# Kernel tuning notes

Measured on AMD Instinct MI355X. Metric: run time of the kernel, lower is better.

The kernel has to match this reference:

```python
import jax, jax.numpy as jnp
import numpy as np

D_MODEL = 40; N_LAYER = 256
D_INNER = 80; D_STATE = 16; D_CONV = 4; DT_RANK = 3  # mamba defaults: expand=2, dt_rank=ceil(40/16)
PE_HID = 48; FF_MULT = 4
B, L, N = 1, 400, 65536


def setup_inputs():
    key = jax.random.key(0)
    ks = jax.random.split(key, 16)
    f32 = jnp.float32
    def rn(k, shape, s=0.02):
        return jax.random.normal(k, shape, f32) * s
    inp = {}
    inp['mash_params'] = jax.random.normal(ks[0], (B, L, D_MODEL), f32)
    inp['qry'] = jax.random.uniform(ks[1], (B, N, 3), f32, -1.0, 1.0)
    # stacked per-layer Mamba params (leading dim = N_LAYER)
    inp['l_norm_w'] = jnp.ones((N_LAYER, D_MODEL), f32)
    inp['l_in_w'] = rn(ks[2], (N_LAYER, 2 * D_INNER, D_MODEL), 0.05)
    inp['l_conv_w'] = rn(ks[3], (N_LAYER, D_INNER, D_CONV), 0.2)
    inp['l_conv_b'] = jnp.zeros((N_LAYER, D_INNER), f32)
    inp['l_xproj_w'] = rn(ks[4], (N_LAYER, DT_RANK + 2 * D_STATE, D_INNER), 0.05)
    inp['l_dt_w'] = rn(ks[5], (N_LAYER, D_INNER, DT_RANK), 0.2)
    inp['l_dt_b'] = rn(ks[6], (N_LAYER, D_INNER), 0.5) - 4.0  # softplus -> small dt
    A = jnp.tile(jnp.arange(1, D_STATE + 1, dtype=f32)[None, None, :], (N_LAYER, D_INNER, 1))
    inp['l_A_log'] = jnp.log(A)
    inp['l_D'] = jnp.ones((N_LAYER, D_INNER), f32)
    inp['l_out_w'] = rn(ks[7], (N_LAYER, D_MODEL, D_INNER), 0.05)
    # PointEmbed MLP (Fourier basis is a fixed buffer, built in forward)
    inp['pe_mlp_w'] = rn(ks[8], (D_MODEL, PE_HID + 3), 0.1)
    inp['pe_mlp_b'] = jnp.zeros((D_MODEL,), f32)
    # PreNorm cross-attention (heads=1, dim_head=d_model)
    inp['ca_lnq_w'] = jnp.ones((D_MODEL,), f32); inp['ca_lnq_b'] = jnp.zeros((D_MODEL,), f32)
    inp['ca_lnc_w'] = jnp.ones((D_MODEL,), f32); inp['ca_lnc_b'] = jnp.zeros((D_MODEL,), f32)
    inp['ca_q_w'] = rn(ks[9], (D_MODEL, D_MODEL), 0.1)
    inp['ca_kv_w'] = rn(ks[10], (2 * D_MODEL, D_MODEL), 0.1)
    inp['ca_out_w'] = rn(ks[11], (D_MODEL, D_MODEL), 0.1)
    inp['ca_out_b'] = jnp.zeros((D_MODEL,), f32)
    # PreNorm GEGLU feed-forward
    inp['ff_ln_w'] = jnp.ones((D_MODEL,), f32); inp['ff_ln_b'] = jnp.zeros((D_MODEL,), f32)
    inp['ff_fc1_w'] = rn(ks[12], (2 * FF_MULT * D_MODEL, D_MODEL), 0.1)
    inp['ff_fc1_b'] = jnp.zeros((2 * FF_MULT * D_MODEL,), f32)
    inp['ff_fc2_w'] = rn(ks[13], (D_MODEL, FF_MULT * D_MODEL), 0.1)
    inp['ff_fc2_b'] = jnp.zeros((D_MODEL,), f32)
    inp['out_w'] = rn(ks[14], (1, D_MODEL), 0.1)
    inp['out_b'] = jnp.zeros((1,), f32)
    return inp


def _rmsnorm(x, w, eps=1e-5):
    return x * jax.lax.rsqrt(jnp.mean(x * x, -1, keepdims=True) + eps) * w


def _layernorm(x, w, b, eps=1e-5):
    m = jnp.mean(x, -1, keepdims=True)
    v = jnp.mean((x - m) ** 2, -1, keepdims=True)
    return (x - m) * jax.lax.rsqrt(v + eps) * w + b


def _mamba(u, p):
    # u: [b, l, d_model]
    xz = jnp.einsum('bld,ed->ble', u, p['in_w'])  # [b,l,2*di]
    x, z = jnp.split(xz, 2, -1)
    # depthwise causal conv1d, kernel D_CONV
    xt = jnp.swapaxes(x, 1, 2)  # [b, di, l]
    xc = jax.lax.conv_general_dilated(xt, p['conv_w'][:, None, :], (1,), [(D_CONV - 1, 0)],
                                      feature_group_count=D_INNER)
    x = jax.nn.silu(jnp.swapaxes(xc + p['conv_b'][None, :, None], 1, 2))  # [b,l,di]
    dbc = jnp.einsum('bld,ed->ble', x, p['xproj_w'])  # [b,l,dt_rank+2*ds]
    dtr = dbc[..., :DT_RANK]
    Bm = dbc[..., DT_RANK:DT_RANK + D_STATE]
    Cm = dbc[..., DT_RANK + D_STATE:]
    dt = jax.nn.softplus(jnp.einsum('blr,dr->bld', dtr, p['dt_w']) + p['dt_b'])  # [b,l,di]
    A = -jnp.exp(p['A_log'])  # [di, ds]
    dA = jnp.exp(dt[..., None] * A)                          # [b,l,di,ds]
    dBx = dt[..., None] * Bm[:, :, None, :] * x[..., None]   # [b,l,di,ds]
    def step(h, io):
        a, bx = io
        h = a * h + bx
        return h, h
    h0 = jnp.zeros((u.shape[0], D_INNER, D_STATE), u.dtype)
    _, hs = jax.lax.scan(step, h0, (jnp.moveaxis(dA, 1, 0), jnp.moveaxis(dBx, 1, 0)))
    hs = jnp.moveaxis(hs, 0, 1)  # [b,l,di,ds]
    y = jnp.einsum('blds,bls->bld', hs, Cm) + x * p['D']
    y = y * jax.nn.silu(z)
    return jnp.einsum('bld,ed->ble', y, p['out_w'])


def _forward(mash_params, qry, l_norm_w, l_in_w, l_conv_w, l_conv_b, l_xproj_w, l_dt_w, l_dt_b,
             l_A_log, l_D, l_out_w, pe_mlp_w, pe_mlp_b, ca_lnq_w, ca_lnq_b, ca_lnc_w, ca_lnc_b,
             ca_q_w, ca_kv_w, ca_out_w, ca_out_b, ff_ln_w, ff_ln_b, ff_fc1_w, ff_fc1_b,
             ff_fc2_w, ff_fc2_b, out_w, out_b):
    layer_params = dict(norm_w=l_norm_w, in_w=l_in_w, conv_w=l_conv_w, conv_b=l_conv_b,
                        xproj_w=l_xproj_w, dt_w=l_dt_w, dt_b=l_dt_b, A_log=l_A_log,
                        D=l_D, out_w=l_out_w)
    # Block: residual = x; h = RMSNorm(x); h = Mamba(h); then caller does x = h + residual
    def layer_fn(x, p):
        return x + _mamba(_rmsnorm(x, p['norm_w']), p), None
    x, _ = jax.lax.scan(layer_fn, mash_params, layer_params)
    # PointEmbed: Fourier features with fixed block-diagonal basis
    e = (2.0 ** jnp.arange(PE_HID // 6, dtype=jnp.float32)) * jnp.pi  # [8]
    z0 = jnp.zeros_like(e)
    basis = jnp.stack([jnp.concatenate([e, z0, z0]),
                       jnp.concatenate([z0, e, z0]),
                       jnp.concatenate([z0, z0, e])])  # [3, 24]
    proj = jnp.einsum('bnd,de->bne', qry, basis)
    pe = jnp.concatenate([jnp.sin(proj), jnp.cos(proj), qry], -1)  # [b,n,51]
    q_emb = jnp.einsum('bnf,df->bnd', pe, pe_mlp_w) + pe_mlp_b
    # PreNorm cross-attention (1 head, dim_head = d_model)
    qn = _layernorm(q_emb, ca_lnq_w, ca_lnq_b)
    cn = _layernorm(x, ca_lnc_w, ca_lnc_b)
    q = jnp.einsum('bnd,ed->bne', qn, ca_q_w)
    kv = jnp.einsum('bld,ed->ble', cn, ca_kv_w)
    k, v = jnp.split(kv, 2, -1)
    scale = D_MODEL ** -0.5
    attn = jax.nn.softmax(jnp.einsum('bnd,bld->bnl', q, k) * scale, axis=-1)  # [b,n,l]
    lat = jnp.einsum('bnl,bld->bnd', attn, v)
    lat = jnp.einsum('bnd,ed->bne', lat, ca_out_w) + ca_out_b
    # PreNorm GEGLU feed-forward with residual
    h = _layernorm(lat, ff_ln_w, ff_ln_b)
    a = jnp.einsum('bnd,ed->bne', h, ff_fc1_w) + ff_fc1_b
    x1, g = jnp.split(a, 2, -1)
    ff = jnp.einsum('bnf,df->bnd', x1 * jax.nn.gelu(g, approximate=False), ff_fc2_w) + ff_fc2_b
    lat = lat + ff
    occ = (jnp.einsum('bnd,od->bno', lat, out_w) + out_b)[..., 0]  # [b, n]
    return occ


def reference(mash_params, qry, l_norm_w, l_in_w, l_conv_w, l_conv_b, l_xproj_w, l_dt_w, l_dt_b,
              l_A_log, l_D, l_out_w, pe_mlp_w, pe_mlp_b, ca_lnq_w, ca_lnq_b, ca_lnc_w, ca_lnc_b,
              ca_q_w, ca_kv_w, ca_out_w, ca_out_b, ff_ln_w, ff_ln_b, ff_fc1_w, ff_fc1_b,
              ff_fc2_w, ff_fc2_b, out_w, out_b):
    return _forward(mash_params, qry, l_norm_w, l_in_w, l_conv_w, l_conv_b, l_xproj_w, l_dt_w,
                    l_dt_b, l_A_log, l_D, l_out_w, pe_mlp_w, pe_mlp_b, ca_lnq_w, ca_lnq_b,
                    ca_lnc_w, ca_lnc_b, ca_q_w, ca_kv_w, ca_out_w, ca_out_b, ff_ln_w, ff_ln_b,
                    ff_fc1_w, ff_fc1_b, ff_fc2_w, ff_fc2_b, out_w, out_b)
```

## Files before the change

### kernel.cpp

```cpp
#include <hip/hip_runtime.h>


#define CH 4
#define NCHUNK 100
#define TPB1 320

typedef unsigned long long u64;

__device__ __forceinline__ u64 pack2(float a, float b) {
  return ((u64)__float_as_uint(b) << 32) | (u64)__float_as_uint(a);
}
__device__ __forceinline__ float unplo(u64 a) {
  return __uint_as_float((unsigned)a);
}
__device__ __forceinline__ float unphi(u64 a) {
  return __uint_as_float((unsigned)(a >> 32));
}

__global__ void init_flags(int* __restrict__ flags) {
  int i = blockIdx.x * 256 + threadIdx.x;
  if (i < 256 * 16) flags[i] = 0;
}

__global__ __launch_bounds__(TPB1) void mamba_pipe(
    const float* __restrict__ mash,
    const float* __restrict__ g_norm_w,
    const float* __restrict__ g_in_w,
    const float* __restrict__ g_conv_w,
    const float* __restrict__ g_conv_b,
    const float* __restrict__ g_xp_w,
    const float* __restrict__ g_dt_w,
    const float* __restrict__ g_dt_b,
    const float* __restrict__ g_alog,
    const float* __restrict__ g_D,
    const float* __restrict__ g_out_w,
    float* __restrict__ xb0,
    float* __restrict__ xb1,
    int* __restrict__ flags,
    const float* __restrict__ qry,
    const float* __restrict__ pe_w, const float* __restrict__ pe_b,
    const float* __restrict__ lnq_w, const float* __restrict__ lnq_b,
    const float* __restrict__ qw,
    float* __restrict__ qstore)
{
  const int tid = threadIdx.x;

  if (blockIdx.x >= 256) {
    const int n = (blockIdx.x - 256) * TPB1 + tid;
    if (n < 65536) {
      const float qx = qry[n * 3 + 0], qy = qry[n * 3 + 1], qz = qry[n * 3 + 2];
      float qe[40];
#pragma unroll
      for (int d = 0; d < 40; ++d) qe[d] = pe_b[d];
#pragma unroll 1
      for (int j = 0; j < 8; ++j) {
        float f = 3.14159265358979323846f * (float)(1 << j);
        float sx, cx, sy, cy, sz, cz;
        __sincosf(qx * f, &sx, &cx);
        __sincosf(qy * f, &sy, &cy);
        __sincosf(qz * f, &sz, &cz);
#pragma unroll
        for (int d = 0; d < 40; ++d) {
          const float* r = pe_w + d * 51;
          qe[d] += sx * r[j] + sy * r[j + 8] + sz * r[j + 16]
                 + cx * r[j + 24] + cy * r[j + 32] + cz * r[j + 40];
        }
      }
#pragma unroll
      for (int d = 0; d < 40; ++d) {
        const float* r = pe_w + d * 51;
        qe[d] += qx * r[48] + qy * r[49] + qz * r[50];
      }
      float qn[40];
      {
        float m = 0.f;
#pragma unroll
        for (int d = 0; d < 40; ++d) m += qe[d];
        m *= (1.f / 40.f);
        float var = 0.f;
#pragma unroll
        for (int d = 0; d < 40; ++d) { float dv = qe[d] - m; var += dv * dv; }
        float rstd = rsqrtf(var * (1.f / 40.f) + 1e-5f);
#pragma unroll
        for (int d = 0; d < 40; ++d)
          qn[d] = (qe[d] - m) * rstd * lnq_w[d] + lnq_b[d];
      }
      float q[40];
#pragma unroll
      for (int e = 0; e < 40; ++e) {
        const float* r = qw + e * 40;
        float s = 0.f;
#pragma unroll
        for (int d = 0; d < 40; ++d) s += qn[d] * r[d];
        q[e] = s;
      }
#pragma unroll
      for (int e = 0; e < 40; ++e) qstore[e * 65536 + n] = q[e];
    }
    return;
  }

  const int layer = blockIdx.x;

  __shared__ float xin[160];
  __shared__ float xz[640];
  __shared__ float xs[320];
  __shared__ float dbc[144];
  __shared__ float yb[320];
  __shared__ float xhist[240];

  const int e_in = tid % 160;
  const int tA = tid / 160;
  float w_in_r[40];
  {
    const float4* g = (const float4*)(g_in_w + layer * 6400 + e_in * 40);
    const float4* nw = (const float4*)(g_norm_w + layer * 40);
#pragma unroll
    for (int k = 0; k < 10; ++k) {
      float4 v = g[k];
      float4 n = nw[k];
      w_in_r[4 * k] = v.x * n.x; w_in_r[4 * k + 1] = v.y * n.y;
      w_in_r[4 * k + 2] = v.z * n.z; w_in_r[4 * k + 3] = v.w * n.w;
    }
  }
  const int d_c = tid % 80;
  const int t_c = tid / 80;
  float cw[4]; float cb;
  {
    float4 v = *(const float4*)(g_conv_w + layer * 320 + d_c * 4);
    cw[0] = v.x; cw[1] = v.y; cw[2] = v.z; cw[3] = v.w;
    cb = g_conv_b[layer * 80 + d_c];
  }
  const int halfp = tid & 1;
  const int p_x = tid >> 1;
  const int t_x = p_x / 35, e_x = p_x % 35;
  float w_xp_r[40];
  if (p_x < 140) {
    const float4* g = (const float4*)(g_xp_w + layer * 2800 + e_x * 80 + halfp * 40);
#pragma unroll
    for (int k = 0; k < 10; ++k) {
      float4 v = g[k];
      w_xp_r[4 * k] = v.x; w_xp_r[4 * k + 1] = v.y;
      w_xp_r[4 * k + 2] = v.z; w_xp_r[4 * k + 3] = v.w;
    }
  }
  const int d_ch = tid >> 2;
  const int qq = tid & 3;
  float negA[4], hst[4];
  {
    float4 v = *(const float4*)(g_alog + layer * 1280 + tid * 4);
    negA[0] = -__expf(v.x); negA[1] = -__expf(v.y);
    negA[2] = -__expf(v.z); negA[3] = -__expf(v.w);
    hst[0] = hst[1] = hst[2] = hst[3] = 0.f;
  }
  const float dtw0 = g_dt_w[layer * 240 + d_ch * 3 + 0];
  const float dtw1 = g_dt_w[layer * 240 + d_ch * 3 + 1];
  const float dtw2 = g_dt_w[layer * 240 + d_ch * 3 + 2];
  const float dtb = g_dt_b[layer * 80 + d_ch];
  const float wD = g_D[layer * 80 + d_ch];
  const int p_o = tid >> 1;
  const int t_o = p_o / 40, e_o = p_o % 40;
  float w_out_r[40];
  {
    const float4* g = (const float4*)(g_out_w + layer * 3200 + e_o * 80 + halfp * 40);
#pragma unroll
    for (int k = 0; k < 10; ++k) {
      float4 v = g[k];
      w_out_r[4 * k] = v.x; w_out_r[4 * k + 1] = v.y;
      w_out_r[4 * k + 2] = v.z; w_out_r[4 * k + 3] = v.w;
    }
  }

  for (int i = tid; i < 240; i += TPB1) xhist[i] = 0.f;
  __syncthreads();

  const float* src = (layer == 0) ? mash : ((layer & 1) ? xb0 : xb1);
  float* dst = (layer & 1) ? xb1 : xb0;
  int* flag_prev = flags + (layer - 1) * 16;
  int* flag_cur = flags + layer * 16;

  for (int c = 0; c < NCHUNK; ++c) {
    const int t0 = c * CH;

    if (layer == 0) {
#pragma unroll
      for (int tt = 0; tt < 2; ++tt) {
        const int t = tA + 2 * tt;
        const float4* sp = (const float4*)(src + (t0 + t) * 40);
        float ss = 0.f, sd = 0.f;
#pragma unroll
        for (int k = 0; k < 10; ++k) {
          float4 v = sp[k];
          ss += v.x * v.x + v.y * v.y + v.z * v.z + v.w * v.w;
          sd += w_in_r[4 * k] * v.x + w_in_r[4 * k + 1] * v.y
              + w_in_r[4 * k + 2] * v.z + w_in_r[4 * k + 3] * v.w;
        }
        xz[t * 160 + e_in] = sd * rsqrtf(ss * (1.f / 40.f) + 1e-5f);
      }
      if (tid < 160) xin[tid] = src[t0 * 40 + tid];
    } else {
      while (__hip_atomic_load(flag_prev, __ATOMIC_RELAXED,
                               __HIP_MEMORY_SCOPE_AGENT) <= c)
        __builtin_amdgcn_s_sleep(1);
#pragma unroll
      for (int tt = 0; tt < 2; ++tt) {
        const int t = tA + 2 * tt;
        const u64* sp = (const u64*)(src + (t0 + t) * 40);
        float ss = 0.f, sd = 0.f;
#pragma unroll
        for (int k = 0; k < 20; ++k) {
          u64 a = __hip_atomic_load(sp + k, __ATOMIC_RELAXED,
                                    __HIP_MEMORY_SCOPE_AGENT);
          float v0 = unplo(a), v1 = unphi(a);
          ss += v0 * v0 + v1 * v1;
          sd += w_in_r[2 * k] * v0 + w_in_r[2 * k + 1] * v1;
        }
        xz[t * 160 + e_in] = sd * rsqrtf(ss * (1.f / 40.f) + 1e-5f);
      }
      if (tid < 80) {
        u64 a = __hip_atomic_load((const u64*)(src + t0 * 40) + tid,
                                  __ATOMIC_RELAXED, __HIP_MEMORY_SCOPE_AGENT);
        xin[2 * tid] = unplo(a);
        xin[2 * tid + 1] = unphi(a);
      }
    }
    __syncthreads();

    {
      float acc = cb;
#pragma unroll
      for (int j = 0; j < 4; ++j) {
        int lt = t_c - 3 + j;
        float xv = (lt >= 0) ? xz[lt * 160 + d_c] : xhist[(lt + 3) * 80 + d_c];
        acc += cw[j] * xv;
      }
      xs[t_c * 80 + d_c] = acc / (1.f + __expf(-acc));
    }
    __syncthreads();

    if (p_x < 140) {
      const float4* xp = (const float4*)&xs[t_x * 80 + halfp * 40];
      float s = 0.f;
#pragma unroll
      for (int k = 0; k < 10; ++k) {
        float4 v = xp[k];
        s += w_xp_r[4 * k] * v.x + w_xp_r[4 * k + 1] * v.y
           + w_xp_r[4 * k + 2] * v.z + w_xp_r[4 * k + 3] * v.w;
      }
      s += __shfl_xor(s, 1);
      if (halfp == 0) dbc[t_x * 36 + e_x] = s;
    } else {
      for (int k = tid - 280; k < 240; k += 40)
        xhist[k] = xz[(1 + k / 80) * 160 + (k % 80)];
    }
    __syncthreads();

#pragma unroll
    for (int t = 0; t < CH; ++t) {
      const float* db = &dbc[t * 36];
      float sdt = dtb + db[0] * dtw0 + db[1] * dtw1 + db[2] * dtw2;
      float dtval = (sdt > 15.f) ? sdt : __logf(1.f + __expf(sdt));
      float xval = xs[t * 80 + d_ch];
      float part = 0.f;
#pragma unroll
      for (int j = 0; j < 4; ++j) {
        int s_i = qq * 4 + j;
        float Bv = db[3 + s_i];
        float Cv = db[19 + s_i];
        hst[j] = __expf(dtval * negA[j]) * hst[j] + dtval * Bv * xval;
        part += hst[j] * Cv;
      }
      part += __shfl_xor(part, 1);
      part += __shfl_xor(part, 2);
      if (qq == 0) {
        float yv = part + xval * wD;
        float z = xz[t * 160 + 80 + d_ch];
        yb[t * 80 + d_ch] = yv * z / (1.f + __expf(-z));
      }
    }
    __syncthreads();

    {
      const float4* yp = (const float4*)&yb[t_o * 80 + halfp * 40];
      float s = 0.f;
#pragma unroll
      for (int k = 0; k < 10; ++k) {
        float4 v = yp[k];
        s += w_out_r[4 * k] * v.x + w_out_r[4 * k + 1] * v.y
           + w_out_r[4 * k + 2] * v.z + w_out_r[4 * k + 3] * v.w;
      }
      s += __shfl_xor(s, 1);
      float r = xin[p_o] + s;
      float r2 = __shfl_xor(r, 2);
      if ((tid & 3) == 0)
        __hip_atomic_store((u64*)(dst + t0 * 40 + p_o), pack2(r, r2),
                           __ATOMIC_RELAXED, __HIP_MEMORY_SCOPE_AGENT);
    }
    __syncthreads();
    if (tid == 0)
      __hip_atomic_store(flag_cur, c + 1, __ATOMIC_RELAXED,
                         __HIP_MEMORY_SCOPE_AGENT);
  }
}

__global__ __launch_bounds__(64) void kv_kernel(
    const float* __restrict__ xfin,
    const float* __restrict__ lnc_w, const float* __restrict__ lnc_b,
    const float* __restrict__ kv_w,
    float* __restrict__ kbuf, float* __restrict__ vbuf)
{
  int t = blockIdx.x;
  int lane = threadIdx.x;
  float x = (lane < 40) ? xfin[t * 40 + lane] : 0.f;
  float s = x;
#pragma unroll
  for (int o = 32; o >= 1; o >>= 1) s += __shfl_xor(s, o);
  float m = s * (1.f / 40.f);
  float dv = (lane < 40) ? (x - m) : 0.f;
  float v2 = dv * dv;
#pragma unroll
  for (int o = 32; o >= 1; o >>= 1) v2 += __shfl_xor(v2, o);
  float rstd = rsqrtf(v2 * (1.f / 40.f) + 1e-5f);
  __shared__ float cn[40];
  if (lane < 40) cn[lane] = dv * rstd * lnc_w[lane] + lnc_b[lane];
  __syncthreads();
  for (int e = lane; e < 80; e += 64) {
    float acc = 0.f;
#pragma unroll
    for (int d = 0; d < 40; ++d) acc += cn[d] * kv_w[e * 40 + d];
    if (e < 40) kbuf[t * 40 + e] = acc;
    else vbuf[t * 40 + (e - 40)] = acc;
  }
}

__global__ __launch_bounds__(256) void query_fast(
    const float* __restrict__ qstore,
    const float* __restrict__ ow, const float* __restrict__ ob,
    const float* __restrict__ flw, const float* __restrict__ flb,
    const float* __restrict__ w1, const float* __restrict__ b1,
    const float* __restrict__ w2, const float* __restrict__ b2,
    const float* __restrict__ outw, const float* __restrict__ outb,
    const float* __restrict__ kbuf, const float* __restrict__ vbuf,
    float* __restrict__ out)
{
  const int tid = threadIdx.x;
  const int h = __builtin_amdgcn_readfirstlane((tid >> 6) & 3);
  const int lane = tid & 63;
  const int n = blockIdx.x * 64 + lane;
  const int p1 = tid ^ 64, p2 = tid ^ 128, p3 = tid ^ 192;
  __shared__ float colbuf[40 * 256];

  float q[40];
#pragma unroll
  for (int e = 0; e < 40; ++e) q[e] = qstore[e * 65536 + n];

  float acc[40];
#pragma unroll
  for (int d = 0; d < 40; ++d) acc[d] = 0.f;
  float mx = -1e30f, l = 0.f;
  const float scale = 0.15811388300841897f;
  const int tbeg = h * 100;
#pragma unroll 1
  for (int t = tbeg; t < tbeg + 100; t += 2) {
    const float4* ka = (const float4*)(kbuf + t * 40);
    const float4* kb = (const float4*)(kbuf + t * 40 + 40);
    float a0 = 0.f, a1 = 0.f, b0 = 0.f, b1s = 0.f;
#pragma unroll
    for (int k = 0; k < 10; ++k) {
      float4 k4 = ka[k];
      float4 j4 = kb[k];
      a0 += q[4 * k] * k4.x + q[4 * k + 1] * k4.y;
      a1 += q[4 * k + 2] * k4.z + q[4 * k + 3] * k4.w;
      b0 += q[4 * k] * j4.x + q[4 * k + 1] * j4.y;
      b1s += q[4 * k + 2] * j4.z + q[4 * k + 3] * j4.w;
    }
    float sa = (a0 + a1) * scale;
    float sb = (b0 + b1s) * scale;
    {
      if (sa > mx) {
        float corr = __expf(mx - sa);
        l *= corr;
#pragma unroll
        for (int d = 0; d < 40; ++d) acc[d] *= corr;
        mx = sa;
      }
      float p = __expf(sa - mx);
      l += p;
      const float4* vr = (const float4*)(vbuf + t * 40);
#pragma unroll
      for (int k = 0; k < 10; ++k) {
        float4 v4 = vr[k];
        acc[4 * k] += p * v4.x; acc[4 * k + 1] += p * v4.y;
        acc[4 * k + 2] += p * v4.z; acc[4 * k + 3] += p * v4.w;
      }
    }
    {
      if (sb > mx) {
        float corr = __expf(mx - sb);
        l *= corr;
#pragma unroll
        for (int d = 0; d < 40; ++d) acc[d] *= corr;
        mx = sb;
      }
      float p = __expf(sb - mx);
      l += p;
      const float4* vr = (const float4*)(vbuf + (t + 1) * 40);
#pragma unroll
      for (int k = 0; k < 10; ++k) {
        float4 v4 = vr[k];
        acc[4 * k] += p * v4.x; acc[4 * k + 1] += p * v4.y;
        acc[4 * k + 2] += p * v4.z; acc[4 * k + 3] += p * v4.w;
      }
    }
  }

  {
    float* redm = colbuf;
    float* redl = colbuf + 256;
    redm[tid] = mx; redl[tid] = l;
  }
  __syncthreads();
  float a0c, a1c, a2c, a3c, linv;
  {
    float m1 = colbuf[p1], m2 = colbuf[p2], m3 = colbuf[p3];
    float l1 = colbuf[256 + p1], l2 = colbuf[256 + p2], l3 = colbuf[256 + p3];
    float nm = fmaxf(fmaxf(mx, m1), fmaxf(m2, m3));
    a0c = __expf(mx - nm); a1c = __expf(m1 - nm);
    a2c = __expf(m2 - nm); a3c = __expf(m3 - nm);
    float L = l * a0c + l1 * a1c + l2 * a2c + l3 * a3c;
    linv = 1.f / L;
  }
  __syncthreads();
#pragma unroll
  for (int d = 0; d < 40; ++d) colbuf[d * 256 + tid] = acc[d];
  __syncthreads();
  float lat[40];
#pragma unroll
  for (int d = 0; d < 40; ++d)
    lat[d] = (acc[d] * a0c + colbuf[d * 256 + p1] * a1c
            + colbuf[d * 256 + p2] * a2c + colbuf[d * 256 + p3] * a3c) * linv;
  __syncthreads();

  float lath[10];
#pragma unroll
  for (int dd = 0; dd < 10; ++dd) {
    float v = lat[dd];
    v = (h == 1) ? lat[dd + 10] : v;
    v = (h == 2) ? lat[dd + 20] : v;
    v = (h == 3) ? lat[dd + 30] : v;
    lath[dd] = v;
  }
  float lp[40];
#pragma unroll
  for (int e = 0; e < 40; ++e) lp[e] = 0.f;
#pragma unroll 1
  for (int dd = 0; dd < 10; ++dd) {
    const float lv = lath[dd];
    const int d = h * 10 + dd;
#pragma unroll
    for (int e = 0; e < 40; ++e) lp[e] += lv * ow[e * 40 + d];
  }
#pragma unroll
  for (int e = 0; e < 40; ++e) colbuf[e * 256 + tid] = lp[e];
  __syncthreads();
  float lat2[40];
#pragma unroll
  for (int e = 0; e < 40; ++e)
    lat2[e] = ob[e] + lp[e] + colbuf[e * 256 + p1]
            + colbuf[e * 256 + p2] + colbuf[e * 256 + p3];
  __syncthreads();

  float hh[40];
  {
    float m = 0.f;
#pragma unroll
    for (int d = 0; d < 40; ++d) m += lat2[d];
    m *= (1.f / 40.f);
    float var = 0.f;
#pragma unroll
    for (int d = 0; d < 40; ++d) { float dv = lat2[d] - m; var += dv * dv; }
    float rstd = rsqrtf(var * (1.f / 40.f) + 1e-5f);
#pragma unroll
    for (int d = 0; d < 40; ++d) hh[d] = (lat2[d] - m) * rstd * flw[d] + flb[d];
  }
  float ff[40];
#pragma unroll
  for (int d = 0; d < 40; ++d) ff[d] = 0.f;
#pragma unroll 1
  for (int ee = 0; ee < 40; ++ee) {
    const int e = h * 40 + ee;
    const float* r1 = w1 + e * 40;
    const float* r2 = w1 + (160 + e) * 40;
    float s0 = 0.f, s1 = 0.f;
#pragma unroll
    for (int d = 0; d < 40; ++d) { s0 += hh[d] * r1[d]; s1 += hh[d] * r2[d]; }
    float x1 = s0 + b1[e];
    float g = s1 + b1[160 + e];
    float tv = x1 * (0.5f * g * (1.f + erff(g * 0.70710678118654752f)));
#pragma unroll
    for (int d = 0; d < 40; ++d) ff[d] += tv * w2[d * 160 + e];
  }
#pragma unroll
  for (int d = 0; d < 40; ++d) colbuf[d * 256 + tid] = ff[d];
  __syncthreads();
  float r = outb[0];
#pragma unroll
  for (int d = 0; d < 40; ++d) {
    float f = ff[d] + colbuf[d * 256 + p1] + colbuf[d * 256 + p2]
            + colbuf[d * 256 + p3] + b2[d];
    r += (lat2[d] + f) * outw[d];
  }
  if (h == 0) out[n] = r;
}

__global__ __launch_bounds__(256) void query_kernel_fb(
    const float* __restrict__ qry,
    const float* __restrict__ pe_w, const float* __restrict__ pe_b,
    const float* __restrict__ lnq_w, const float* __restrict__ lnq_b,
    const float* __restrict__ qw,
    const float* __restrict__ ow, const float* __restrict__ ob,
    const float* __restrict__ flw, const float* __restrict__ flb,
    const float* __restrict__ w1, const float* __restrict__ b1,
    const float* __restrict__ w2, const float* __restrict__ b2,
    const float* __restrict__ outw, const float* __restrict__ outb,
    const float* __restrict__ kbuf, const float* __restrict__ vbuf,
    float* __restrict__ out)
{
  const int tid = threadIdx.x;
  const int h = __builtin_amdgcn_readfirstlane((tid >> 6) & 1);
  const int pj = tid >> 7;
  const int lane = tid & 63;
  const int n = blockIdx.x * 128 + pj * 64 + lane;
  const int ptn = tid ^ 64;
  __shared__ float colbuf[40 * 256];
  __shared__ float redm[256], redl[256];

  const float qx = qry[n * 3 + 0], qy = qry[n * 3 + 1], qz = qry[n * 3 + 2];
  float qp[40];
#pragma unroll
  for (int d = 0; d < 40; ++d) qp[d] = 0.f;
#pragma unroll
  for (int jj = 0; jj < 4; ++jj) {
    const int j = h * 4 + jj;
    float f = 3.14159265358979323846f * (float)(1 << j);
    float sx, cx, sy, cy, sz, cz;
    __sincosf(qx * f, &sx, &cx);
    __sincosf(qy * f, &sy, &cy);
    __sincosf(qz * f, &sz, &cz);
#pragma unroll
    for (int d = 0; d < 40; ++d) {
      const float* r = pe_w + d * 51;
      qp[d] += sx * r[j] + sy * r[j + 8] + sz * r[j + 16]
             + cx * r[j + 24] + cy * r[j + 32] + cz * r[j + 40];
    }
  }
#pragma unroll
  for (int d = 0; d < 40; ++d) colbuf[d * 256 + tid] = qp[d];
  __syncthreads();
  float qe[40];
#pragma unroll
  for (int d = 0; d < 40; ++d) {
    const float* r = pe_w + d * 51;
    qe[d] = pe_b[d] + qp[d] + colbuf[d * 256 + ptn]
          + qx * r[48] + qy * r[49] + qz * r[50];
  }
  __syncthreads();
  float qn[40];
  {
    float m = 0.f;
#pragma unroll
    for (int d = 0; d < 40; ++d) m += qe[d];
    m *= (1.f / 40.f);
    float var = 0.f;
#pragma unroll
    for (int d = 0; d < 40; ++d) { float dv = qe[d] - m; var += dv * dv; }
    float rstd = rsqrtf(var * (1.f / 40.f) + 1e-5f);
#pragma unroll
    for (int d = 0; d < 40; ++d) qn[d] = (qe[d] - m) * rstd * lnq_w[d] + lnq_b[d];
  }
  float qnh[20];
#pragma unroll
  for (int dd = 0; dd < 20; ++dd) qnh[dd] = h ? qn[dd + 20] : qn[dd];
  float q[40];
#pragma unroll
  for (int e = 0; e < 40; ++e) q[e] = 0.f;
#pragma unroll 1
  for (int dd = 0; dd < 20; ++dd) {
    const float qv = qnh[dd];
    const int d = h * 20 + dd;
#pragma unroll
    for (int e = 0; e < 40; ++e) q[e] += qv * qw[e * 40 + d];
  }
#pragma unroll
  for (int e = 0; e < 40; ++e) colbuf[e * 256 + tid] = q[e];
  __syncthreads();
#pragma unroll
  for (int e = 0; e < 40; ++e) q[e] += colbuf[e * 256 + ptn];
  __syncthreads();

  float acc[40];
#pragma unroll
  for (int d = 0; d < 40; ++d) acc[d] = 0.f;
  float mx = -1e30f, l = 0.f;
  const float scale = 0.15811388300841897f;
  const int tbeg = h * 200, tend = tbeg + 200;
#pragma unroll 1
  for (int t = tbeg; t < tend; ++t) {
    const float4* kr = (const float4*)(kbuf + t * 40);
    float s0 = 0.f, s1 = 0.f, s2 = 0.f, s3 = 0.f;
#pragma unroll
    for (int k = 0; k < 10; ++k) {
      float4 k4 = kr[k];
      s0 += q[4 * k] * k4.x; s1 += q[4 * k + 1] * k4.y;
      s2 += q[4 * k + 2] * k4.z; s3 += q[4 * k + 3] * k4.w;
    }
    float s = ((s0 + s1) + (s2 + s3)) * scale;
    if (s > mx) {
      float corr = __expf(mx - s);
      l *= corr;
#pragma unroll
      for (int d = 0; d < 40; ++d) acc[d] *= corr;
      mx = s;
    }
    float p = __expf(s - mx);
    l += p;
    const float4* vr = (const float4*)(vbuf + t * 40);
#pragma unroll
    for (int k = 0; k < 10; ++k) {
      float4 v4 = vr[k];
      acc[4 * k] += p * v4.x; acc[4 * k + 1] += p * v4.y;
      acc[4 * k + 2] += p * v4.z; acc[4 * k + 3] += p * v4.w;
    }
  }
#pragma unroll
  for (int d = 0; d < 40; ++d) colbuf[d * 256 + tid] = acc[d];
  redm[tid] = mx; redl[tid] = l;
  __syncthreads();
  float lat[40];
  {
    float m2 = redm[ptn];
    float l2 = redl[ptn];
    float nm = fmaxf(mx, m2);
    float a = __expf(mx - nm), b = __expf(m2 - nm);
    float lm = l * a + l2 * b;
    float linv = 1.f / lm;
#pragma unroll
    for (int d = 0; d < 40; ++d)
      lat[d] = (acc[d] * a + colbuf[d * 256 + ptn] * b) * linv;
  }
  __syncthreads();
  float lath[20];
#pragma unroll
  for (int dd = 0; dd < 20; ++dd) lath[dd] = h ? lat[dd + 20] : lat[dd];
  float lp[40];
#pragma unroll
  for (int e = 0; e < 40; ++e) lp[e] = 0.f;
#pragma unroll 1
  for (int dd = 0; dd < 20; ++dd) {
    const float lv = lath[dd];
    const int d = h * 20 + dd;
#pragma unroll
    for (int e = 0; e < 40; ++e) lp[e] += lv * ow[e * 40 + d];
  }
#pragma unroll
  for (int e = 0; e < 40; ++e) colbuf[e * 256 + tid] = lp[e];
  __syncthreads();
  float lat2[40];
#pragma unroll
  for (int e = 0; e < 40; ++e) lat2[e] = ob[e] + lp[e] + colbuf[e * 256 + ptn];
  __syncthreads();
  float hh[40];
  {
    float m = 0.f;
#pragma unroll
    for (int d = 0; d < 40; ++d) m += lat2[d];
    m *= (1.f / 40.f);
    float var = 0.f;
#pragma unroll
    for (int d = 0; d < 40; ++d) { float dv = lat2[d] - m; var += dv * dv; }
    float rstd = rsqrtf(var * (1.f / 40.f) + 1e-5f);
#pragma unroll
    for (int d = 0; d < 40; ++d) hh[d] = (lat2[d] - m) * rstd * flw[d] + flb[d];
  }
  float ff[40];
#pragma unroll
  for (int d = 0; d < 40; ++d) ff[d] = 0.f;
#pragma unroll 1
  for (int ee = 0; ee < 80; ++ee) {
    const int e = h * 80 + ee;
    const float* r1 = w1 + e * 40;
    const float* r2 = w1 + (160 + e) * 40;
    float s0 = 0.f, s1 = 0.f;
#pragma unroll
    for (int d = 0; d < 40; ++d) { s0 += hh[d] * r1[d]; s1 += hh[d] * r2[d]; }
    float x1 = s0 + b1[e];
    float g = s1 + b1[160 + e];
    float tv = x1 * (0.5f * g * (1.f + erff(g * 0.70710678118654752f)));
#pragma unroll
    for (int d = 0; d < 40; ++d) ff[d] += tv * w2[d * 160 + e];
  }
#pragma unroll
  for (int d = 0; d < 40; ++d) colbuf[d * 256 + tid] = ff[d];
  __syncthreads();
  float r = outb[0];
#pragma unroll
  for (int d = 0; d < 40; ++d) {
    float f = ff[d] + colbuf[d * 256 + ptn] + b2[d];
    r += (lat2[d] + f) * outw[d];
  }
  if (h == 0) out[n] = r;
}

extern "C" void kernel_launch(void* const* d_in, const int* in_sizes, int n_in,
                              void* d_out, int out_size, void* d_ws, size_t ws_size,
                              hipStream_t stream) {
  const float* mash   = (const float*)d_in[0];
  const float* qry    = (const float*)d_in[1];
  const float* lnw    = (const float*)d_in[2];
  const float* linw   = (const float*)d_in[3];
  const float* lconvw = (const float*)d_in[4];
  const float* lconvb = (const float*)d_in[5];
  const float* lxpw   = (const float*)d_in[6];
  const float* ldtw   = (const float*)d_in[7];
  const float* ldtb   = (const float*)d_in[8];
  const float* lAlog  = (const float*)d_in[9];
  const float* lD     = (const float*)d_in[10];
  const float* loutw  = (const float*)d_in[11];
  const float* pew    = (const float*)d_in[12];
  const float* peb    = (const float*)d_in[13];
  const float* lnqw   = (const float*)d_in[14];
  const float* lnqb   = (const float*)d_in[15];
  const float* lncw   = (const float*)d_in[16];
  const float* lncb   = (const float*)d_in[17];
  const float* qw     = (const float*)d_in[18];
  const float* kvw    = (const float*)d_in[19];
  const float* oww    = (const float*)d_in[20];
  const float* owb    = (const float*)d_in[21];
  const float* flnw   = (const float*)d_in[22];
  const float* flnb   = (const float*)d_in[23];
  const float* w1     = (const float*)d_in[24];
  const float* b1     = (const float*)d_in[25];
  const float* w2     = (const float*)d_in[26];
  const float* b2     = (const float*)d_in[27];
  const float* outw   = (const float*)d_in[28];
  const float* outb   = (const float*)d_in[29];

  float* wsf = (float*)d_ws;
  float* xb0 = wsf;
  float* xb1 = wsf + 16000;
  float* kbuf = wsf + 32000;
  float* vbuf = wsf + 48000;
  int* flags = (int*)(wsf + 64000);
  float* qstore = wsf + 68096;
  const size_t needed = (size_t)68096 * 4 + (size_t)40 * 65536 * 4;
  const bool pre = ws_size >= needed;

  hipLaunchKernelGGL(init_flags, dim3(16), dim3(256), 0, stream, flags);
  hipLaunchKernelGGL(mamba_pipe, dim3(pre ? 461 : 256), dim3(TPB1), 0, stream,
                     mash, lnw, linw, lconvw, lconvb, lxpw, ldtw, ldtb, lAlog,
                     lD, loutw, xb0, xb1, flags,
                     qry, pew, peb, lnqw, lnqb, qw, qstore);
  hipLaunchKernelGGL(kv_kernel, dim3(400), dim3(64), 0, stream,
                     xb1, lncw, lncb, kvw, kbuf, vbuf);
  if (pre) {
    hipLaunchKernelGGL(query_fast, dim3(1024), dim3(256), 0, stream,
                       qstore, oww, owb, flnw, flnb,
                       w1, b1, w2, b2, outw, outb, kbuf, vbuf, (float*)d_out);
  } else {
    hipLaunchKernelGGL(query_kernel_fb, dim3(512), dim3(256), 0, stream,
                       qry, pew, peb, lnqw, lnqb, qw, oww, owb, flnw, flnb,
                       w1, b1, w2, b2, outw, outb, kbuf, vbuf, (float*)d_out);
  }
}
```

Baseline: 2.113 ms.

## Fuse KV projection and query attention into the Mamba pipeline via flag-driven streaming

Adds 205 extra blocks to the persistent mamba_pipe kernel. They wait until point-embedding blocks publish q, then consume each final-layer output chunk as soon as its flag advances, computing LayerNorm and the K/V projection on the fly and running online-softmax attention and the feed-forward tail per query. This removes the separate kv_kernel and query_fast launches and overlaps query work with the serial 256-layer scan. In exchange it relies on spin-waiting blocks being co-resident with the producer blocks. Each thread also now does the whole FFN and output projection alone rather than splitting it across four waves, so per-thread compute rises.

Result: no change. 2.151 ms (+1.8%).

```diff
diff --git a/kernel.cpp b/kernel.cpp
--- a/kernel.cpp
+++ b/kernel.cpp
@@ -4,6 +4,8 @@
 #define CH 4
 #define NCHUNK 100
 #define TPB1 320
+#define NPE 205
+#define NQA 205
 
 typedef unsigned long long u64;
 
@@ -41,11 +43,19 @@
     const float* __restrict__ pe_w, const float* __restrict__ pe_b,
     const float* __restrict__ lnq_w, const float* __restrict__ lnq_b,
     const float* __restrict__ qw,
-    float* __restrict__ qstore)
+    float* __restrict__ qstore,
+    const float* __restrict__ lnc_w, const float* __restrict__ lnc_b,
+    const float* __restrict__ kv_w,
+    const float* __restrict__ ow, const float* __restrict__ ob,
+    const float* __restrict__ flw, const float* __restrict__ flb,
+    const float* __restrict__ w1, const float* __restrict__ b1,
+    const float* __restrict__ w2, const float* __restrict__ b2,
+    const float* __restrict__ outw, const float* __restrict__ outb,
+    float* __restrict__ out)
 {
   const int tid = threadIdx.x;
 
-  if (blockIdx.x >= 256) {
+  if (blockIdx.x >= 256 && blockIdx.x < 256 + NPE) {
     const int n = (blockIdx.x - 256) * TPB1 + tid;
     if (n < 65536) {
       const float qx = qry[n * 3 + 0], qy = qry[n * 3 + 1], qz = qry[n * 3 + 2];
@@ -95,8 +105,162 @@
         q[e] = s;
       }
 #pragma unroll
-      for (int e = 0; e < 40; ++e) qstore[e * 65536 + n] = q[e];
-    }
+      for (int e = 0; e < 40; ++e)
+        __hip_atomic_store(&qstore[e * 65536 + n], q[e],
+                           __ATOMIC_RELAXED, __HIP_MEMORY_SCOPE_AGENT);
+    }
+    __syncthreads();
+    if (tid == 0)
+      __hip_atomic_fetch_add(flags + 4088, 1,
+                             __ATOMIC_RELAXED, __HIP_MEMORY_SCOPE_AGENT);
+    return;
+  }
+
+  if (blockIdx.x >= 256 + NPE) {
+    const int n = (blockIdx.x - 256 - NPE) * TPB1 + tid;
+    const bool qvalid = (n < 65536);
+    const int w = tid >> 6;
+    const int lane = tid & 63;
+    __shared__ __align__(16) float kvx[160];
+    __shared__ __align__(16) float cns[4][40];
+    __shared__ __align__(16) float ks[4][40];
+    __shared__ __align__(16) float vs[4][40];
+
+    int* pe_done = flags + 4088;
+    int* flag255 = flags + 255 * 16;
+
+    while (__hip_atomic_load(pe_done, __ATOMIC_RELAXED,
+                             __HIP_MEMORY_SCOPE_AGENT) < NPE)
+      __builtin_amdgcn_s_sleep(32);
+
+    float q[40];
+#pragma unroll
+    for (int e = 0; e < 40; ++e)
+      q[e] = qvalid ? __hip_atomic_load(&qstore[e * 65536 + n],
+                                        __ATOMIC_RELAXED,
+                                        __HIP_MEMORY_SCOPE_AGENT) : 0.f;
+
+    float acc[40];
+#pragma unroll
+    for (int d = 0; d < 40; ++d) acc[d] = 0.f;
+    float mx = -1e30f, l = 0.f;
+    const float scale = 0.15811388300841897f;
+
+#pragma unroll 1
+    for (int c = 0; c < NCHUNK; ++c) {
+      while (__hip_atomic_load(flag255, __ATOMIC_RELAXED,
+                               __HIP_MEMORY_SCOPE_AGENT) <= c)
+        __builtin_amdgcn_s_sleep(32);
+      if (tid < 80) {
+        u64 a = __hip_atomic_load((const u64*)(xb1 + c * 160) + tid,
+                                  __ATOMIC_RELAXED, __HIP_MEMORY_SCOPE_AGENT);
+        kvx[2 * tid] = unplo(a);
+        kvx[2 * tid + 1] = unphi(a);
+      }
+      __syncthreads();
+      {
+        float x = (w < 4 && lane < 40) ? kvx[w * 40 + lane] : 0.f;
+        float s = x;
+#pragma unroll
+        for (int o = 32; o >= 1; o >>= 1) s += __shfl_xor(s, o);
+        float m = s * (1.f / 40.f);
+        float dv = (lane < 40) ? (x - m) : 0.f;
+        float v2 = dv * dv;
+#pragma unroll
+        for (int o = 32; o >= 1; o >>= 1) v2 += __shfl_xor(v2, o);
+        float rstd = rsqrtf(v2 * (1.f / 40.f) + 1e-5f);
+        if (w < 4 && lane < 40)
+          cns[w][lane] = dv * rstd * lnc_w[lane] + lnc_b[lane];
+      }
+      __syncthreads();
+      if (w < 4) {
+        for (int e = lane; e < 80; e += 64) {
+          float a = 0.f;
+#pragma unroll
+          for (int d = 0; d < 40; ++d) a += cns[w][d] * kv_w[e * 40 + d];
+          if (e < 40) ks[w][e] = a;
+          else vs[w][e - 40] = a;
+        }
+      }
+      __syncthreads();
+#pragma unroll 1
+      for (int t = 0; t < 4; ++t) {
+        const float4* kr = (const float4*)&ks[t][0];
+        float s0 = 0.f, s1 = 0.f, s2 = 0.f, s3 = 0.f;
+#pragma unroll
+        for (int k = 0; k < 10; ++k) {
+          float4 k4 = kr[k];
+          s0 += q[4 * k] * k4.x; s1 += q[4 * k + 1] * k4.y;
+          s2 += q[4 * k + 2] * k4.z; s3 += q[4 * k + 3] * k4.w;
+        }
+        float s = ((s0 + s1) + (s2 + s3)) * scale;
+        if (s > mx) {
+          float corr = __expf(mx - s);
+          l *= corr;
+#pragma unroll
+          for (int d = 0; d < 40; ++d) acc[d] *= corr;
+          mx = s;
+        }
+        float p = __expf(s - mx);
+        l += p;
+        const float4* vr = (const float4*)&vs[t][0];
+#pragma unroll
+        for (int k = 0; k < 10; ++k) {
+          float4 v4 = vr[k];
+          acc[4 * k] += p * v4.x; acc[4 * k + 1] += p * v4.y;
+          acc[4 * k + 2] += p * v4.z; acc[4 * k + 3] += p * v4.w;
+        }
+      }
+      __syncthreads();
+    }
+
+    float linv = 1.f / l;
+#pragma unroll
+    for (int d = 0; d < 40; ++d) acc[d] *= linv;
+    float lat2[40];
+#pragma unroll 1
+    for (int e = 0; e < 40; ++e) {
+      const float* r = ow + e * 40;
+      float s = 0.f;
+#pragma unroll
+      for (int d = 0; d < 40; ++d) s += acc[d] * r[d];
+      lat2[e] = ob[e] + s;
+    }
+    float hh[40];
+    {
+      float m = 0.f;
+#pragma unroll
+      for (int d = 0; d < 40; ++d) m += lat2[d];
+      m *= (1.f / 40.f);
+      float var = 0.f;
+#pragma unroll
+      for (int d = 0; d < 40; ++d) { float dv = lat2[d] - m; var += dv * dv; }
+      float rstd = rsqrtf(var * (1.f / 40.f) + 1e-5f);
+#pragma unroll
+      for (int d = 0; d < 40; ++d)
+        hh[d] = (lat2[d] - m) * rstd * flw[d] + flb[d];
+    }
+    float ff[40];
+#pragma unroll
+    for (int d = 0; d < 40; ++d) ff[d] = 0.f;
+#pragma unroll 1
+    for (int e = 0; e < 160; ++e) {
+      const float* r1 = w1 + e * 40;
+      const float* r2 = w1 + (160 + e) * 40;
+      float s0 = 0.f, s1 = 0.f;
+#pragma unroll
+      for (int d = 0; d < 40; ++d) { s0 += hh[d] * r1[d]; s1 += hh[d] * r2[d]; }
+      float x1 = s0 + b1[e];
+      float g = s1 + b1[160 + e];
+      float tv = x1 * (0.5f * g * (1.f + erff(g * 0.70710678118654752f)));
+#pragma unroll
+      for (int d = 0; d < 40; ++d) ff[d] += tv * w2[d * 160 + e];
+    }
+    float r = outb[0];
+#pragma unroll
+    for (int d = 0; d < 40; ++d)
+      r += (lat2[d] + ff[d] + b2[d]) * outw[d];
+    if (qvalid) out[n] = r;
     return;
   }
 
@@ -331,186 +495,6 @@
     if (e < 40) kbuf[t * 40 + e] = acc;
     else vbuf[t * 40 + (e - 40)] = acc;
   }
-}
-
-__global__ __launch_bounds__(256) void query_fast(
-    const float* __restrict__ qstore,
-    const float* __restrict__ ow, const float* __restrict__ ob,
-    const float* __restrict__ flw, const float* __restrict__ flb,
-    const float* __restrict__ w1, const float* __restrict__ b1,
-    const float* __restrict__ w2, const float* __restrict__ b2,
-    const float* __restrict__ outw, const float* __restrict__ outb,
-    const float* __restrict__ kbuf, const float* __restrict__ vbuf,
-    float* __restrict__ out)
-{
-  const int tid = threadIdx.x;
-  const int h = __builtin_amdgcn_readfirstlane((tid >> 6) & 3);
-  const int lane = tid & 63;
-  const int n = blockIdx.x * 64 + lane;
-  const int p1 = tid ^ 64, p2 = tid ^ 128, p3 = tid ^ 192;
-  __shared__ float colbuf[40 * 256];
-
-  float q[40];
-#pragma unroll
-  for (int e = 0; e < 40; ++e) q[e] = qstore[e * 65536 + n];
-
-  float acc[40];
-#pragma unroll
-  for (int d = 0; d < 40; ++d) acc[d] = 0.f;
-  float mx = -1e30f, l = 0.f;
-  const float scale = 0.15811388300841897f;
-  const int tbeg = h * 100;
-#pragma unroll 1
-  for (int t = tbeg; t < tbeg + 100; t += 2) {
-    const float4* ka = (const float4*)(kbuf + t * 40);
-    const float4* kb = (const float4*)(kbuf + t * 40 + 40);
-    float a0 = 0.f, a1 = 0.f, b0 = 0.f, b1s = 0.f;
-#pragma unroll
-    for (int k = 0; k < 10; ++k) {
-      float4 k4 = ka[k];
-      float4 j4 = kb[k];
-      a0 += q[4 * k] * k4.x + q[4 * k + 1] * k4.y;
-      a1 += q[4 * k + 2] * k4.z + q[4 * k + 3] * k4.w;
-      b0 += q[4 * k] * j4.x + q[4 * k + 1] * j4.y;
-      b1s += q[4 * k + 2] * j4.z + q[4 * k + 3] * j4.w;
-    }
-    float sa = (a0 + a1) * scale;
-    float sb = (b0 + b1s) * scale;
-    {
-      if (sa > mx) {
-        float corr = __expf(mx - sa);
-        l *= corr;
-#pragma unroll
-        for (int d = 0; d < 40; ++d) acc[d] *= corr;
-        mx = sa;
-      }
-      float p = __expf(sa - mx);
-      l += p;
-      const float4* vr = (const float4*)(vbuf + t * 40);
-#pragma unroll
-      for (int k = 0; k < 10; ++k) {
-        float4 v4 = vr[k];
-        acc[4 * k] += p * v4.x; acc[4 * k + 1] += p * v4.y;
-        acc[4 * k + 2] += p * v4.z; acc[4 * k + 3] += p * v4.w;
-      }
-    }
-    {
-      if (sb > mx) {
-        float corr = __expf(mx - sb);
-        l *= corr;
-#pragma unroll
-        for (int d = 0; d < 40; ++d) acc[d] *= corr;
-        mx = sb;
-      }
-      float p = __expf(sb - mx);
-      l += p;
-      const float4* vr = (const float4*)(vbuf + (t + 1) * 40);
-#pragma unroll
-      for (int k = 0; k < 10; ++k) {
-        float4 v4 = vr[k];
-        acc[4 * k] += p * v4.x; acc[4 * k + 1] += p * v4.y;
-        acc[4 * k + 2] += p * v4.z; acc[4 * k + 3] += p * v4.w;
-      }
-    }
-  }
-
-  {
-    float* redm = colbuf;
-    float* redl = colbuf + 256;
-    redm[tid] = mx; redl[tid] = l;
-  }
-  __syncthreads();
-  float a0c, a1c, a2c, a3c, linv;
-  {
-    float m1 = colbuf[p1], m2 = colbuf[p2], m3 = colbuf[p3];
-    float l1 = colbuf[256 + p1], l2 = colbuf[256 + p2], l3 = colbuf[256 + p3];
-    float nm = fmaxf(fmaxf(mx, m1), fmaxf(m2, m3));
-    a0c = __expf(mx - nm); a1c = __expf(m1 - nm);
-    a2c = __expf(m2 - nm); a3c = __expf(m3 - nm);
-    float L = l * a0c + l1 * a1c + l2 * a2c + l3 * a3c;
-    linv = 1.f / L;
-  }
-  __syncthreads();
-#pragma unroll
-  for (int d = 0; d < 40; ++d) colbuf[d * 256 + tid] = acc[d];
-  __syncthreads();
-  float lat[40];
-#pragma unroll
-  for (int d = 0; d < 40; ++d)
-    lat[d] = (acc[d] * a0c + colbuf[d * 256 + p1] * a1c
-            + colbuf[d * 256 + p2] * a2c + colbuf[d * 256 + p3] * a3c) * linv;
-  __syncthreads();
-
-  float lath[10];
-#pragma unroll
-  for (int dd = 0; dd < 10; ++dd) {
-    float v = lat[dd];
-    v = (h == 1) ? lat[dd + 10] : v;
-    v = (h == 2) ? lat[dd + 20] : v;
-    v = (h == 3) ? lat[dd + 30] : v;
-    lath[dd] = v;
-  }
-  float lp[40];
-#pragma unroll
-  for (int e = 0; e < 40; ++e) lp[e] = 0.f;
-#pragma unroll 1
-  for (int dd = 0; dd < 10; ++dd) {
-    const float lv = lath[dd];
-    const int d = h * 10 + dd;
-#pragma unroll
-    for (int e = 0; e < 40; ++e) lp[e] += lv * ow[e * 40 + d];
-  }
-#pragma unroll
-  for (int e = 0; e < 40; ++e) colbuf[e * 256 + tid] = lp[e];
-  __syncthreads();
-  float lat2[40];
-#pragma unroll
-  for (int e = 0; e < 40; ++e)
-    lat2[e] = ob[e] + lp[e] + colbuf[e * 256 + p1]
-            + colbuf[e * 256 + p2] + colbuf[e * 256 + p3];
-  __syncthreads();
-
-  float hh[40];
-  {
-    float m = 0.f;
-#pragma unroll
-    for (int d = 0; d < 40; ++d) m += lat2[d];
-    m *= (1.f / 40.f);
-    float var = 0.f;
-#pragma unroll
-    for (int d = 0; d < 40; ++d) { float dv = lat2[d] - m; var += dv * dv; }
-    float rstd = rsqrtf(var * (1.f / 40.f) + 1e-5f);
-#pragma unroll
-    for (int d = 0; d < 40; ++d) hh[d] = (lat2[d] - m) * rstd * flw[d] + flb[d];
-  }
-  float ff[40];
-#pragma unroll
-  for (int d = 0; d < 40; ++d) ff[d] = 0.f;
-#pragma unroll 1
-  for (int ee = 0; ee < 40; ++ee) {
-    const int e = h * 40 + ee;
-    const float* r1 = w1 + e * 40;
-    const float* r2 = w1 + (160 + e) * 40;
-    float s0 = 0.f, s1 = 0.f;
-#pragma unroll
-    for (int d = 0; d < 40; ++d) { s0 += hh[d] * r1[d]; s1 += hh[d] * r2[d]; }
-    float x1 = s0 + b1[e];
-    float g = s1 + b1[160 + e];
-    float tv = x1 * (0.5f * g * (1.f + erff(g * 0.70710678118654752f)));
-#pragma unroll
-    for (int d = 0; d < 40; ++d) ff[d] += tv * w2[d * 160 + e];
-  }
-#pragma unroll
-  for (int d = 0; d < 40; ++d) colbuf[d * 256 + tid] = ff[d];
-  __syncthreads();
-  float r = outb[0];
-#pragma unroll
-  for (int d = 0; d < 40; ++d) {
-    float f = ff[d] + colbuf[d * 256 + p1] + colbuf[d * 256 + p2]
-            + colbuf[d * 256 + p3] + b2[d];
-    r += (lat2[d] + f) * outw[d];
-  }
-  if (h == 0) out[n] = r;
 }
 
 __global__ __launch_bounds__(256) void query_kernel_fb(
@@ -756,17 +740,16 @@
   const bool pre = ws_size >= needed;
 
   hipLaunchKernelGGL(init_flags, dim3(16), dim3(256), 0, stream, flags);
-  hipLaunchKernelGGL(mamba_pipe, dim3(pre ? 461 : 256), dim3(TPB1), 0, stream,
+  hipLaunchKernelGGL(mamba_pipe, dim3(pre ? 256 + NPE + NQA : 256), dim3(TPB1),
+                     0, stream,
                      mash, lnw, linw, lconvw, lconvb, lxpw, ldtw, ldtb, lAlog,
                      lD, loutw, xb0, xb1, flags,
-                     qry, pew, peb, lnqw, lnqb, qw, qstore);
-  hipLaunchKernelGGL(kv_kernel, dim3(400), dim3(64), 0, stream,
-                     xb1, lncw, lncb, kvw, kbuf, vbuf);
-  if (pre) {
-    hipLaunchKernelGGL(query_fast, dim3(1024), dim3(256), 0, stream,
-                       qstore, oww, owb, flnw, flnb,
-                       w1, b1, w2, b2, outw, outb, kbuf, vbuf, (float*)d_out);
-  } else {
+                     qry, pew, peb, lnqw, lnqb, qw, qstore,
+                     lncw, lncb, kvw, oww, owb, flnw, flnb,
+                     w1, b1, w2, b2, outw, outb, (float*)d_out);
+  if (!pre) {
+    hipLaunchKernelGGL(kv_kernel, dim3(400), dim3(64), 0, stream,
+                       xb1, lncw, lncb, kvw, kbuf, vbuf);
     hipLaunchKernelGGL(query_kernel_fb, dim3(512), dim3(256), 0, stream,
                        qry, pew, peb, lnqw, lnqb, qw, oww, owb, flnw, flnb,
                        w1, b1, w2, b2, outw, outb, kbuf, vbuf, (float*)d_out);
```
